# Performance work log

Hardware: AMD Instinct MI355X
Metric: run time of the kernel (lower is better)

## Reference

```python
import jax, jax.numpy as jnp
import numpy as np

R, D, H, NLAYERS = 128, 64, 64, 3
B, N = 64, 1024
INIT_W = 0.1


def setup_inputs() -> dict:
    key = jax.random.key(0)
    ks = jax.random.split(key, 10)
    x = jax.random.normal(ks[0], (B, D, N), dtype=jnp.float32)
    L = jax.random.randint(ks[1], (B, 1, N), 0, 2, dtype=jnp.int32)
    wq0 = INIT_W * jax.random.normal(ks[2], (R, D), dtype=jnp.float32)
    wqr = INIT_W * jax.random.normal(ks[3], (NLAYERS - 1, R, R), dtype=jnp.float32)
    wk0 = INIT_W * jax.random.normal(ks[4], (R, D), dtype=jnp.float32)
    wkr = INIT_W * jax.random.normal(ks[5], (NLAYERS - 1, R, R), dtype=jnp.float32)
    wv0 = INIT_W * jax.random.normal(ks[6], (R, D), dtype=jnp.float32)
    wvr = INIT_W * jax.random.normal(ks[7], (NLAYERS - 1, R, R), dtype=jnp.float32)
    wor = INIT_W * jax.random.normal(ks[8], (NLAYERS - 1, R, R), dtype=jnp.float32)
    wo_last = INIT_W * jax.random.normal(ks[9], (H, R), dtype=jnp.float32)
    return {"x": x, "L": L, "wq0": wq0, "wqr": wqr, "wk0": wk0, "wkr": wkr,
            "wv0": wv0, "wvr": wvr, "wor": wor, "wo_last": wo_last}


def reference(x, L, wq0, wqr, wk0, wkr, wv0, wvr, wor, wo_last):
    # x: [B, d, N]; L: [B, 1, N] neighbor mask (first row used)
    Lrow = L[:, 0, :].astype(jnp.float32)                      # [B, N]
    num_neighbors = jnp.sum((Lrow >= 1).astype(jnp.float32), axis=1)[:, None, None] + 1.0  # [B,1,1]
    scale = jnp.sqrt(num_neighbors)
    mask = Lrow[:, None, :]                                    # [B, 1, N], broadcast over r

    inp = x
    for layer in range(NLAYERS):
        Wq = wq0 if layer == 0 else wqr[layer - 1]
        Wk = wk0 if layer == 0 else wkr[layer - 1]
        Wv = wv0 if layer == 0 else wvr[layer - 1]
        # sigmoid-gated projections: [B, r, N]
        Q = jax.nn.sigmoid(jnp.einsum('rd,bdn->brn', Wq, inp))
        K = jax.nn.sigmoid(jnp.einsum('rd,bdn->brn', Wk, inp))
        V = jax.nn.sigmoid(jnp.einsum('rd,bdn->brn', Wv, inp))
        # degree-scaled softmax attention over agents: scores [B, N, N]
        A = jax.nn.softmax(jnp.einsum('brn,brm->bnm', Q, K) / scale, axis=-1)
        # o[b,r,n] = sum_m A[b,n,m] * V[b,r,m]  -> [B, r, N]
        o = jnp.einsum('bnm,brm->brn', A, V)
        Wo = wor[layer] if layer < NLAYERS - 1 else wo_last
        inp = jax.nn.silu(jnp.einsum('or,brn->bon', Wo, o))
        if layer != NLAYERS - 1:  # remask_bias=True
            inp = mask * inp
    return inp  # [B, h, N]
```

## Files before the change

kernel.cpp:

```cpp
#include <hip/hip_runtime.h>


typedef __bf16 bf16;
typedef bf16 bf16x2 __attribute__((ext_vector_type(2)));
typedef bf16 bf16x4 __attribute__((ext_vector_type(4)));
typedef bf16 bf16x8 __attribute__((ext_vector_type(8)));
typedef float f32x4 __attribute__((ext_vector_type(4)));
typedef float f32x16 __attribute__((ext_vector_type(16)));
typedef unsigned int u32;
typedef u32 u32x4 __attribute__((ext_vector_type(4)));

#define MFMA32(a, b, c) __builtin_amdgcn_mfma_f32_32x32x16_bf16(a, b, c, 0, 0, 0)
#define ZERO16 {0,0,0,0,0,0,0,0,0,0,0,0,0,0,0,0}
#define LOG2E 1.44269504f

__device__ __forceinline__ float fast_exp2(float x) {
  return __builtin_amdgcn_exp2f(x);
}
__device__ __forceinline__ float fast_sigmoid(float x) {
  return __builtin_amdgcn_rcpf(1.0f + fast_exp2(-LOG2E * x));
}
__device__ __forceinline__ u32 cvt_pk_bf16(float lo, float hi) {
  u32 r;
  asm("v_cvt_pk_bf16_f32 %0, %1, %2" : "=v"(r) : "v"(lo), "v"(hi));
  return r;
}
__device__ __forceinline__ void pl32_swap(u32& a, u32& b) {
  asm("v_permlane32_swap_b32 %0, %1" : "+v"(a), "+v"(b));
}
__device__ __forceinline__ void build_frags(const f32x16 v, bf16x8& f0, bf16x8& f1) {
  u32 t0 = cvt_pk_bf16(v[0], v[1]);
  u32 t1 = cvt_pk_bf16(v[2], v[3]);
  u32 t2 = cvt_pk_bf16(v[4], v[5]);
  u32 t3 = cvt_pk_bf16(v[6], v[7]);
  pl32_swap(t0, t2);
  pl32_swap(t1, t3);
  u32x4 a = {t0, t1, t2, t3};
  f0 = __builtin_bit_cast(bf16x8, a);
  u32 s0 = cvt_pk_bf16(v[8], v[9]);
  u32 s1 = cvt_pk_bf16(v[10], v[11]);
  u32 s2 = cvt_pk_bf16(v[12], v[13]);
  u32 s3 = cvt_pk_bf16(v[14], v[15]);
  pl32_swap(s0, s2);
  pl32_swap(s1, s3);
  u32x4 c = {s0, s1, s2, s3};
  f1 = __builtin_bit_cast(bf16x8, c);
}
__device__ __forceinline__ float treesum16(const f32x16 v) {
  float a0 = v[0] + v[1], a1 = v[2] + v[3], a2 = v[4] + v[5], a3 = v[6] + v[7];
  float a4 = v[8] + v[9], a5 = v[10] + v[11], a6 = v[12] + v[13], a7 = v[14] + v[15];
  float b0 = a0 + a1, b1 = a2 + a3, b2 = a4 + a5, b3 = a6 + a7;
  return (b0 + b1) + (b2 + b3);
}

__global__ __launch_bounds__(256) void prep_kernel(
    const int* __restrict__ L,
    const float* __restrict__ wq0, const float* __restrict__ wqr,
    const float* __restrict__ wk0, const float* __restrict__ wkr,
    const float* __restrict__ wv0, const float* __restrict__ wvr,
    const float* __restrict__ wor, const float* __restrict__ wo_last,
    float* __restrict__ scale_inv, float* __restrict__ biasv,
    bf16* __restrict__ wbf) {
  __shared__ int red[256];
  const int blk = blockIdx.x;
  const int tid = threadIdx.x;
  if (blk < 64) {
    int cnt = 0;
    for (int n = tid; n < 1024; n += 256) cnt += (L[blk * 1024 + n] >= 1) ? 1 : 0;
    red[tid] = cnt;
    __syncthreads();
    for (int s = 128; s > 0; s >>= 1) {
      if (tid < s) red[tid] += red[tid + s];
      __syncthreads();
    }
    if (tid == 0) {
      float iv = rsqrtf((float)red[0] + 1.0f);
      scale_inv[blk] = iv;
      biasv[blk] = fmaxf(0.0f, 128.0f * iv * LOG2E - 80.0f);
    }
  } else {
    for (int i = (blk - 64) * 256 + tid; i < 163840; i += 64 * 256) {
      float v;
      if      (i <   8192) v = wq0[i];
      else if (i <  40960) v = wqr[i - 8192];
      else if (i <  49152) v = wk0[i - 40960];
      else if (i <  81920) v = wkr[i - 49152];
      else if (i <  90112) v = wv0[i - 81920];
      else if (i < 122880) v = wvr[i - 90112];
      else if (i < 155648) v = wor[i - 122880];
      else                 v = wo_last[i - 155648];
      wbf[i] = (bf16)v;
    }
  }
}

__global__ __launch_bounds__(256) void xk0_kernel(
    const float* __restrict__ x, const bf16* __restrict__ Wk,
    const bf16* __restrict__ Wv, bf16* __restrict__ xT,
    bf16* __restrict__ Kt, bf16* __restrict__ Vn) {
  __shared__ float tile[64][65];
  __shared__ __attribute__((aligned(16))) bf16 inp_lds[64 * 72];
  const int tid = threadIdx.x;
  const int lane = tid & 63, wv = tid >> 6;
  const int la = lane & 31, hi = lane >> 5;
  const int b = blockIdx.x >> 4;
  const int t0 = (blockIdx.x & 15) * 64;

  {
    const int nl = tid & 63, dbase = (tid >> 6) * 16;
#pragma unroll
    for (int i = 0; i < 16; i++) {
      int d = dbase + i;
      tile[d][nl] = x[(size_t)(b * 64 + d) * 1024 + t0 + nl];
    }
  }
  __syncthreads();
  {
    const int dl = (tid & 31) * 2, nb = (tid >> 5) * 8;
#pragma unroll
    for (int i = 0; i < 8; i++) {
      int n = nb + i;
      bf16x2 pr = {(bf16)tile[dl][n], (bf16)tile[dl + 1][n]};
      *(bf16x2*)(xT + (size_t)(b * 1024 + t0 + n) * 64 + dl) = pr;
      *(bf16x2*)&inp_lds[n * 72 + dl] = pr;
    }
  }
  __syncthreads();

  const int sub = wv & 1;
  if (wv < 2) {
#pragma unroll
    for (int rt2 = 0; rt2 < 2; rt2++) {
      const int rt = 2 * sub + rt2;
      bf16x8 wf[4];
#pragma unroll
      for (int ks = 0; ks < 4; ks++)
        wf[ks] = *(const bf16x8*)(Wk + (size_t)(la + 32 * rt) * 64 + hi * 8 + ks * 16);
#pragma unroll
      for (int tt = 0; tt < 2; tt++) {
        f32x16 acc = ZERO16;
#pragma unroll
        for (int ks = 0; ks < 4; ks++) {
          bf16x8 bfr = *(const bf16x8*)&inp_lds[(la + 32 * tt) * 72 + hi * 8 + ks * 16];
          acc = MFMA32(wf[ks], bfr, acc);
        }
#pragma unroll
        for (int g = 0; g < 4; g++) {
          bf16x4 pk;
#pragma unroll
          for (int i = 0; i < 4; i++) pk[i] = (bf16)fast_sigmoid(acc[4 * g + i]);
          *(bf16x4*)(Kt + (size_t)(b * 1024 + t0 + 32 * tt + la) * 128 +
                     32 * rt + 8 * g + 4 * hi) = pk;
        }
      }
    }
  } else {
#pragma unroll
    for (int rc2 = 0; rc2 < 2; rc2++) {
      const int rc = 2 * sub + rc2;
      bf16x8 wf[4];
#pragma unroll
      for (int ks = 0; ks < 4; ks++)
        wf[ks] = *(const bf16x8*)(Wv + (size_t)(la + 32 * rc) * 64 + hi * 8 + ks * 16);
#pragma unroll
      for (int tt = 0; tt < 2; tt++) {
        f32x16 acc = ZERO16;
#pragma unroll
        for (int ks = 0; ks < 4; ks++) {
          bf16x8 afr = *(const bf16x8*)&inp_lds[(la + 32 * tt) * 72 + hi * 8 + ks * 16];
          acc = MFMA32(afr, wf[ks], acc);
        }
#pragma unroll
        for (int g = 0; g < 4; g++) {
          bf16x4 pk;
#pragma unroll
          for (int i = 0; i < 4; i++) pk[i] = (bf16)fast_sigmoid(acc[4 * g + i]);
          *(bf16x4*)(Vn + (size_t)(b * 128 + la + 32 * rc) * 1024 +
                     t0 + 32 * tt + 8 * g + 4 * hi) = pk;
        }
      }
    }
  }
}

template <int DIN>
__global__ __launch_bounds__(256) void kv_kernel(
    const bf16* __restrict__ inpT, const bf16* __restrict__ Wk,
    const bf16* __restrict__ Wv, bf16* __restrict__ Kt,
    bf16* __restrict__ Vn) {
  constexpr int SIN = DIN + 8;
  constexpr int KS = DIN / 16;
  constexpr int CPR = DIN / 8;
  __shared__ __attribute__((aligned(16))) bf16 inp_lds[64 * SIN];
  const int tid = threadIdx.x;
  const int lane = tid & 63, wv = tid >> 6;
  const int la = lane & 31, hi = lane >> 5;
  const int b = blockIdx.x >> 4;
  const int t0 = (blockIdx.x & 15) * 64;

  for (int i = tid; i < 64 * CPR; i += 256) {
    int row = i / CPR, c = i % CPR;
    *(bf16x8*)&inp_lds[row * SIN + c * 8] =
        *(const bf16x8*)(inpT + (size_t)(b * 1024 + t0 + row) * DIN + c * 8);
  }
  __syncthreads();

  const int sub = wv & 1;
  if (wv < 2) {
#pragma unroll
    for (int rt2 = 0; rt2 < 2; rt2++) {
      const int rt = 2 * sub + rt2;
      bf16x8 wf[KS];
#pragma unroll
      for (int ks = 0; ks < KS; ks++)
        wf[ks] = *(const bf16x8*)(Wk + (size_t)(la + 32 * rt) * DIN + hi * 8 + ks * 16);
#pragma unroll
      for (int tt = 0; tt < 2; tt++) {
        f32x16 acc = ZERO16;
#pragma unroll
        for (int ks = 0; ks < KS; ks++) {
          bf16x8 bfr = *(const bf16x8*)&inp_lds[(la + 32 * tt) * SIN + hi * 8 + ks * 16];
          acc = MFMA32(wf[ks], bfr, acc);
        }
#pragma unroll
        for (int g = 0; g < 4; g++) {
          bf16x4 pk;
#pragma unroll
          for (int i = 0; i < 4; i++) pk[i] = (bf16)fast_sigmoid(acc[4 * g + i]);
          *(bf16x4*)(Kt + (size_t)(b * 1024 + t0 + 32 * tt + la) * 128 +
                     32 * rt + 8 * g + 4 * hi) = pk;
        }
      }
    }
  } else {
#pragma unroll
    for (int rc2 = 0; rc2 < 2; rc2++) {
      const int rc = 2 * sub + rc2;
      bf16x8 wf[KS];
#pragma unroll
      for (int ks = 0; ks < KS; ks++)
        wf[ks] = *(const bf16x8*)(Wv + (size_t)(la + 32 * rc) * DIN + hi * 8 + ks * 16);
#pragma unroll
      for (int tt = 0; tt < 2; tt++) {
        f32x16 acc = ZERO16;
#pragma unroll
        for (int ks = 0; ks < KS; ks++) {
          bf16x8 afr = *(const bf16x8*)&inp_lds[(la + 32 * tt) * SIN + hi * 8 + ks * 16];
          acc = MFMA32(afr, wf[ks], acc);
        }
#pragma unroll
        for (int g = 0; g < 4; g++) {
          bf16x4 pk;
#pragma unroll
          for (int i = 0; i < 4; i++) pk[i] = (bf16)fast_sigmoid(acc[4 * g + i]);
          *(bf16x4*)(Vn + (size_t)(b * 128 + 32 * rc + la) * 1024 +
                     t0 + 32 * tt + 8 * g + 4 * hi) = pk;
        }
      }
    }
  }
}

template <int DIN>
__global__ __launch_bounds__(256, 2) void flash_kernel(
    const bf16* __restrict__ inpT, const bf16* __restrict__ Wq,
    const bf16* __restrict__ Kt, const bf16* __restrict__ Vn,
    const float* __restrict__ scale_inv, const float* __restrict__ biasv,
    const int* __restrict__ L, const bf16* __restrict__ Wo,
    void* __restrict__ outp, int last,
    const bf16* __restrict__ Wkn, const bf16* __restrict__ Wvn,
    bf16* __restrict__ Ktn, bf16* __restrict__ Vnn, int kvgen) {
  __shared__ __attribute__((aligned(16))) char smem[71680];

  const int tid = threadIdx.x;
  const int lane = tid & 63, wv = tid >> 6;
  const int la = lane & 31, hi = lane >> 5;
  const int xcd = blockIdx.x & 7;
  const int kk = blockIdx.x >> 3;
  const int b = xcd * 8 + (kk & 7);
  const int q0 = (kk >> 3) * 128;

  const float inv2 = scale_inv[b] * LOG2E;
  const float bb = biasv[b];

  const int krow = tid >> 4, kc = (tid & 15) * 8;
  const int vrow = tid >> 3, vc = (tid & 7) * 8;
  const bf16* kbase = Kt + (size_t)b * 1024 * 128;
  const bf16* vbase = Vn + (size_t)b * 128 * 1024;

  bf16x8 kr[4], vr[4];
#pragma unroll
  for (int p = 0; p < 4; p++) {
    kr[p] = *(const bf16x8*)(kbase + (size_t)(krow + 16 * p) * 128 + kc);
    vr[p] = *(const bf16x8*)(vbase + (size_t)(vrow + 32 * p) * 1024 + vc);
  }

  bf16x8 qB[8];
  {
    constexpr int SIN = DIN + 8;
    constexpr int KSD = DIN / 16;
    constexpr int CPR = DIN / 8;
    bf16* inp_s = (bf16*)smem;
    for (int i = tid; i < 128 * CPR; i += 256) {
      int row = i / CPR, c = i % CPR;
      *(bf16x8*)&inp_s[row * SIN + c * 8] =
          *(const bf16x8*)(inpT + (size_t)(b * 1024 + q0 + row) * DIN + c * 8);
    }
    __syncthreads();
    bf16x8 bfr[KSD];
#pragma unroll
    for (int ks = 0; ks < KSD; ks++)
      bfr[ks] = *(const bf16x8*)&inp_s[(32 * wv + la) * SIN + hi * 8 + ks * 16];
#pragma unroll
    for (int rt = 0; rt < 4; rt++) {
      f32x16 acc = ZERO16;
#pragma unroll
      for (int ks = 0; ks < KSD; ks++) {
        bf16x8 wf = *(const bf16x8*)(Wq + (size_t)(32 * rt + la) * DIN +
                                     hi * 8 + ks * 16);
        acc = MFMA32(wf, bfr[ks], acc);
      }
      f32x16 qv;
#pragma unroll
      for (int j = 0; j < 16; j++) qv[j] = fast_sigmoid(acc[j]) * inv2;
      build_frags(qv, qB[2 * rt], qB[2 * rt + 1]);
    }
    __syncthreads();
  }

  {
    bf16* K0 = (bf16*)smem;
    bf16* V0 = (bf16*)(smem + 34816);
#pragma unroll
    for (int p = 0; p < 4; p++) *(bf16x8*)&K0[(krow + 16 * p) * 136 + kc] = kr[p];
#pragma unroll
    for (int p = 0; p < 4; p++) *(bf16x8*)&V0[(vrow + 32 * p) * 72 + vc] = vr[p];
#pragma unroll
    for (int p = 0; p < 4; p++) {
      kr[p] = *(const bf16x8*)(kbase + (size_t)(64 + krow + 16 * p) * 128 + kc);
      vr[p] = *(const bf16x8*)(vbase + (size_t)(vrow + 32 * p) * 1024 + 64 + vc);
    }
    __syncthreads();
  }

  f32x16 acc_o[4] = {ZERO16, ZERO16, ZERO16, ZERO16};
  float rs = 0.f;

  for (int it = 0; it < 16; it++) {
    const int cur = it & 1;
    const bf16* Kc = (const bf16*)(smem + cur * 17408);
    const bf16* Vc = (const bf16*)(smem + 34816 + cur * 18432);
    if (it < 15) {
      bf16* Kn = (bf16*)(smem + (1 - cur) * 17408);
      bf16* Vx = (bf16*)(smem + 34816 + (1 - cur) * 18432);
#pragma unroll
      for (int p = 0; p < 4; p++)
        *(bf16x8*)&Kn[(krow + 16 * p) * 136 + kc] = kr[p];
#pragma unroll
      for (int p = 0; p < 4; p++)
        *(bf16x8*)&Vx[(vrow + 32 * p) * 72 + vc] = vr[p];
    }
    if (it < 14) {
      const int m2 = (it + 2) * 64;
#pragma unroll
      for (int p = 0; p < 4; p++) {
        kr[p] = *(const bf16x8*)(kbase + (size_t)(m2 + krow + 16 * p) * 128 + kc);
        vr[p] = *(const bf16x8*)(vbase + (size_t)(vrow + 32 * p) * 1024 + m2 + vc);
      }
    }

    f32x16 s00 = ZERO16, s01 = ZERO16, s10 = ZERO16, s11 = ZERO16;
    __builtin_amdgcn_s_setprio(1);
#pragma unroll
    for (int ks = 0; ks < 4; ks++) {
      bf16x8 k0a = *(const bf16x8*)&Kc[la * 136 + hi * 8 + ks * 16];
      s00 = MFMA32(k0a, qB[ks], s00);
      bf16x8 k0b = *(const bf16x8*)&Kc[la * 136 + hi * 8 + (ks + 4) * 16];
      s01 = MFMA32(k0b, qB[ks + 4], s01);
      bf16x8 k1a = *(const bf16x8*)&Kc[(32 + la) * 136 + hi * 8 + ks * 16];
      s10 = MFMA32(k1a, qB[ks], s10);
      bf16x8 k1b = *(const bf16x8*)&Kc[(32 + la) * 136 + hi * 8 + (ks + 4) * 16];
      s11 = MFMA32(k1b, qB[ks + 4], s11);
    }
    __builtin_amdgcn_s_setprio(0);

    bf16x8 pa[4];
    {
      f32x16 pv;
#pragma unroll
      for (int j = 0; j < 16; j++) pv[j] = fast_exp2(s00[j] + s01[j] - bb);
      rs += treesum16(pv);
      build_frags(pv, pa[0], pa[1]);
    }
    {
      f32x16 pv;
#pragma unroll
      for (int j = 0; j < 16; j++) pv[j] = fast_exp2(s10[j] + s11[j] - bb);
      rs += treesum16(pv);
      build_frags(pv, pa[2], pa[3]);
    }

    __builtin_amdgcn_s_setprio(1);
#pragma unroll
    for (int rt = 0; rt < 4; rt++) {
#pragma unroll
      for (int k2 = 0; k2 < 4; k2++) {
        bf16x8 vB = *(const bf16x8*)&Vc[(32 * rt + la) * 72 + hi * 8 + k2 * 16];
        acc_o[rt] = MFMA32(pa[k2], vB, acc_o[rt]);
      }
    }
    __builtin_amdgcn_s_setprio(0);
    __syncthreads();
  }

  rs += __shfl_xor(rs, 32, 64);
  float* rsp = (float*)(smem + 34816);
  if (lane < 32) rsp[32 * wv + la] = rs;
  bf16* O_lds = (bf16*)smem;
#pragma unroll
  for (int g = 0; g < 4; g++) {
    const int qb = 8 * g + 4 * hi;
    f32x4 r4 = *(f32x4*)&rsp[32 * wv + qb];
    f32x4 is;
#pragma unroll
    for (int i = 0; i < 4; i++) is[i] = 1.0f / r4[i];
#pragma unroll
    for (int rt = 0; rt < 4; rt++) {
#pragma unroll
      for (int i = 0; i < 4; i++) {
        O_lds[(size_t)(32 * wv + qb + i) * 136 + 32 * rt + la] =
            (bf16)(acc_o[rt][4 * g + i] * is[i]);
      }
    }
  }
  __syncthreads();

  if (!last) {
    bf16* out_b = (bf16*)outp;
    bf16* O2 = (bf16*)(smem + 36864);
    const int* Lg = L + b * 1024 + q0;
    bf16x8 wB[8];
#pragma unroll
    for (int ks = 0; ks < 8; ks++)
      wB[ks] = *(const bf16x8*)(Wo + (size_t)(la + 32 * wv) * 128 + hi * 8 + ks * 16);
#pragma unroll
    for (int nt = 0; nt < 4; nt++) {
      f32x16 acc = ZERO16;
#pragma unroll
      for (int ks = 0; ks < 8; ks++) {
        bf16x8 oA = *(const bf16x8*)&O_lds[(size_t)(la + 32 * nt) * 136 +
                                           hi * 8 + ks * 16];
        acc = MFMA32(oA, wB[ks], acc);
      }
#pragma unroll
      for (int g = 0; g < 4; g++) {
#pragma unroll
        for (int i = 0; i < 4; i++) {
          int n = 32 * nt + 8 * g + 4 * hi + i;
          float xv = acc[4 * g + i];
          float y = xv * fast_sigmoid(xv) * (float)Lg[n];
          out_b[(size_t)(b * 1024 + q0 + n) * 128 + 32 * wv + la] = (bf16)y;
          if (kvgen) O2[(size_t)n * 136 + 32 * wv + la] = (bf16)y;
        }
      }
    }
    if (kvgen) {
      __syncthreads();
      const bf16* O2c = (const bf16*)(smem + 36864);
      const int sub = wv & 1;
      const bf16* W2 = (wv < 2) ? Wkn : Wvn;
#pragma unroll
      for (int rt2 = 0; rt2 < 2; rt2++) {
        const int rt = 2 * sub + rt2;
        bf16x8 wf[8];
#pragma unroll
        for (int ks = 0; ks < 8; ks++)
          wf[ks] = *(const bf16x8*)(W2 + (size_t)(la + 32 * rt) * 128 +
                                    hi * 8 + ks * 16);
#pragma unroll
        for (int tt = 0; tt < 4; tt++) {
          f32x16 acc = ZERO16;
          if (wv < 2) {
#pragma unroll
            for (int ks = 0; ks < 8; ks++) {
              bf16x8 bB = *(const bf16x8*)&O2c[(size_t)(32 * tt + la) * 136 +
                                               hi * 8 + ks * 16];
              acc = MFMA32(wf[ks], bB, acc);
            }
#pragma unroll
            for (int g = 0; g < 4; g++) {
              bf16x4 pk;
#pragma unroll
              for (int i = 0; i < 4; i++) pk[i] = (bf16)fast_sigmoid(acc[4 * g + i]);
              *(bf16x4*)(Ktn + (size_t)(b * 1024 + q0 + 32 * tt + la) * 128 +
                         32 * rt + 8 * g + 4 * hi) = pk;
            }
          } else {
#pragma unroll
            for (int ks = 0; ks < 8; ks++) {
              bf16x8 aA = *(const bf16x8*)&O2c[(size_t)(32 * tt + la) * 136 +
                                               hi * 8 + ks * 16];
              acc = MFMA32(aA, wf[ks], acc);
            }
#pragma unroll
            for (int g = 0; g < 4; g++) {
              bf16x4 pk;
#pragma unroll
              for (int i = 0; i < 4; i++) pk[i] = (bf16)fast_sigmoid(acc[4 * g + i]);
              *(bf16x4*)(Vnn + (size_t)(b * 128 + 32 * rt + la) * 1024 +
                         q0 + 32 * tt + 8 * g + 4 * hi) = pk;
            }
          }
        }
      }
    }
  } else {
    const int hs = wv & 1, nq = wv >> 1;
    float* outf = (float*)outp;
    bf16x8 wA[8];
#pragma unroll
    for (int ks = 0; ks < 8; ks++)
      wA[ks] = *(const bf16x8*)(Wo + (size_t)(la + 32 * hs) * 128 + hi * 8 + ks * 16);
#pragma unroll
    for (int t = 0; t < 2; t++) {
      const int ns4 = nq + 2 * t;
      f32x16 acc = ZERO16;
#pragma unroll
      for (int ks = 0; ks < 8; ks++) {
        bf16x8 oB = *(const bf16x8*)&O_lds[(size_t)(32 * ns4 + la) * 136 +
                                           hi * 8 + ks * 16];
        acc = MFMA32(wA[ks], oB, acc);
      }
#pragma unroll
      for (int g = 0; g < 4; g++) {
#pragma unroll
        for (int i = 0; i < 4; i++) {
          int h = 32 * hs + 8 * g + 4 * hi + i;
          float xv = acc[4 * g + i];
          outf[(size_t)(b * 64 + h) * 1024 + q0 + 32 * ns4 + la] =
              xv * fast_sigmoid(xv);
        }
      }
    }
  }
}

__global__ __launch_bounds__(256) void xpose_kernel(const float* __restrict__ x,
                                                    bf16* __restrict__ xT) {
  __shared__ float tile[64][65];
  const int blk = blockIdx.x;
  const int b = blk >> 4;
  const int n0 = (blk & 15) * 64;
  const int tid = threadIdx.x;
  {
    const int nl = tid & 63, dbase = (tid >> 6) * 16;
#pragma unroll
    for (int i = 0; i < 16; i++) {
      int d = dbase + i;
      tile[d][nl] = x[(size_t)(b * 64 + d) * 1024 + n0 + nl];
    }
  }
  __syncthreads();
  {
    const int dl = (tid & 31) * 2, nb = (tid >> 5) * 8;
#pragma unroll
    for (int i = 0; i < 8; i++) {
      int n = nb + i;
      bf16x2 pr = {(bf16)tile[dl][n], (bf16)tile[dl + 1][n]};
      *(bf16x2*)(xT + (size_t)(b * 1024 + n0 + n) * 64 + dl) = pr;
    }
  }
}

extern "C" void kernel_launch(void* const* d_in, const int* in_sizes, int n_in,
                              void* d_out, int out_size, void* d_ws, size_t ws_size,
                              hipStream_t stream) {
  const float* x = (const float*)d_in[0];
  const int* L = (const int*)d_in[1];
  const float* wq0 = (const float*)d_in[2];
  const float* wqr = (const float*)d_in[3];
  const float* wk0 = (const float*)d_in[4];
  const float* wkr = (const float*)d_in[5];
  const float* wv0 = (const float*)d_in[6];
  const float* wvr = (const float*)d_in[7];
  const float* wor = (const float*)d_in[8];
  const float* wo_last = (const float*)d_in[9];

  char* ws = (char*)d_ws;
  float* scale_inv = (float*)(ws + 0);
  float* biasv = (float*)(ws + 1024);
  bf16* wbf = (bf16*)(ws + 4096);
  bf16* xT = (bf16*)(ws + 335872);
  bf16* inpT = (bf16*)(ws + 8724480);
  bf16* KtA = (bf16*)(ws + 25501696);
  bf16* VnA = (bf16*)(ws + 42278912);
  bf16* KtB = (bf16*)(ws + 59056128);
  bf16* VnB = (bf16*)(ws + 75833344);

  prep_kernel<<<128, 256, 0, stream>>>(L, wq0, wqr, wk0, wkr, wv0, wvr, wor,
                                       wo_last, scale_inv, biasv, wbf);

  if (ws_size >= 92610560) {
    xk0_kernel<<<1024, 256, 0, stream>>>(x, wbf + 40960, wbf + 81920, xT, KtA, VnA);
    flash_kernel<64><<<512, 256, 0, stream>>>(
        xT, wbf + 0, KtA, VnA, scale_inv, biasv, L, wbf + 122880, (void*)inpT, 0,
        wbf + 49152, wbf + 90112, KtB, VnB, 1);
    flash_kernel<128><<<512, 256, 0, stream>>>(
        inpT, wbf + 8192, KtB, VnB, scale_inv, biasv, L, wbf + 139264,
        (void*)inpT, 0, wbf + 65536, wbf + 106496, KtA, VnA, 1);
    flash_kernel<128><<<512, 256, 0, stream>>>(
        inpT, wbf + 24576, KtA, VnA, scale_inv, biasv, L, wbf + 155648, d_out, 1,
        nullptr, nullptr, nullptr, nullptr, 0);
  } else if (ws_size >= 59056128) {
    xpose_kernel<<<1024, 256, 0, stream>>>(x, xT);
    for (int l = 0; l < 3; l++) {
      const bf16* Wq = (l == 0) ? wbf + 0 : wbf + 8192 + (size_t)(l - 1) * 16384;
      const bf16* Wk = (l == 0) ? wbf + 40960 : wbf + 49152 + (size_t)(l - 1) * 16384;
      const bf16* Wv = (l == 0) ? wbf + 81920 : wbf + 90112 + (size_t)(l - 1) * 16384;
      const bf16* Wo = (l < 2) ? wbf + 122880 + (size_t)l * 16384 : wbf + 155648;
      void* outp = (l < 2) ? (void*)inpT : (void*)d_out;
      if (l == 0) {
        kv_kernel<64><<<1024, 256, 0, stream>>>(xT, Wk, Wv, KtA, VnA);
        flash_kernel<64><<<512, 256, 0, stream>>>(xT, Wq, KtA, VnA, scale_inv,
                                                  biasv, L, Wo, outp, 0,
                                                  nullptr, nullptr, nullptr,
                                                  nullptr, 0);
      } else {
        kv_kernel<128><<<1024, 256, 0, stream>>>(inpT, Wk, Wv, KtA, VnA);
        flash_kernel<128><<<512, 256, 0, stream>>>(inpT, Wq, KtA, VnA, scale_inv,
                                                   biasv, L, Wo, outp,
                                                   (l == 2) ? 1 : 0, nullptr,
                                                   nullptr, nullptr, nullptr, 0);
      }
    }
  }
}
```

Baseline: 272.5 us.

## Load K fragments directly from global into registers, bypassing LDS staging

Each wave now reads its K MFMA fragments straight from global memory into registers (kfA/kfB) instead of staging K tiles through double-buffered LDS. The next tile's loads are issued after the softmax step so they overlap with the P·V MFMAs. This removes the LDS writes and reads for K and frees LDS, so the shared-memory regions are remapped and one barrier is dropped. The QK score accumulation is also merged into one 8-deep accumulator chain per row half instead of two split chains. In exchange, all four waves fetch the same K data from global/L2, and about 64 extra VGPRs are needed, which could hurt occupancy.

```diff
diff --git a/kernel.cpp b/kernel.cpp
--- a/kernel.cpp
+++ b/kernel.cpp
@@ -283,24 +283,24 @@
   const float inv2 = scale_inv[b] * LOG2E;
   const float bb = biasv[b];
 
-  const int krow = tid >> 4, kc = (tid & 15) * 8;
   const int vrow = tid >> 3, vc = (tid & 7) * 8;
   const bf16* kbase = Kt + (size_t)b * 1024 * 128;
   const bf16* vbase = Vn + (size_t)b * 128 * 1024;
 
-  bf16x8 kr[4], vr[4];
-#pragma unroll
-  for (int p = 0; p < 4; p++) {
-    kr[p] = *(const bf16x8*)(kbase + (size_t)(krow + 16 * p) * 128 + kc);
+  bf16x8 vr[4];
+#pragma unroll
+  for (int p = 0; p < 4; p++)
     vr[p] = *(const bf16x8*)(vbase + (size_t)(vrow + 32 * p) * 1024 + vc);
-  }
+
+  const bf16* ka0 = kbase + (size_t)la * 128 + hi * 8;
+  const bf16* ka1 = kbase + (size_t)(32 + la) * 128 + hi * 8;
 
   bf16x8 qB[8];
   {
     constexpr int SIN = DIN + 8;
     constexpr int KSD = DIN / 16;
     constexpr int CPR = DIN / 8;
-    bf16* inp_s = (bf16*)smem;
+    bf16* inp_s = (bf16*)(smem + 36864);
     for (int i = tid; i < 128 * CPR; i += 256) {
       int row = i / CPR, c = i % CPR;
       *(bf16x8*)&inp_s[row * SIN + c * 8] =
@@ -325,20 +325,21 @@
       for (int j = 0; j < 16; j++) qv[j] = fast_sigmoid(acc[j]) * inv2;
       build_frags(qv, qB[2 * rt], qB[2 * rt + 1]);
     }
-    __syncthreads();
-  }
-
+  }
+
+  bf16x8 kfA[8], kfB[8];
   {
-    bf16* K0 = (bf16*)smem;
-    bf16* V0 = (bf16*)(smem + 34816);
-#pragma unroll
-    for (int p = 0; p < 4; p++) *(bf16x8*)&K0[(krow + 16 * p) * 136 + kc] = kr[p];
-#pragma unroll
-    for (int p = 0; p < 4; p++) *(bf16x8*)&V0[(vrow + 32 * p) * 72 + vc] = vr[p];
-#pragma unroll
-    for (int p = 0; p < 4; p++) {
-      kr[p] = *(const bf16x8*)(kbase + (size_t)(64 + krow + 16 * p) * 128 + kc);
+    bf16* V0 = (bf16*)smem;
+#pragma unroll
+    for (int p = 0; p < 4; p++)
+      *(bf16x8*)&V0[(vrow + 32 * p) * 72 + vc] = vr[p];
+#pragma unroll
+    for (int p = 0; p < 4; p++)
       vr[p] = *(const bf16x8*)(vbase + (size_t)(vrow + 32 * p) * 1024 + 64 + vc);
+#pragma unroll
+    for (int ks = 0; ks < 8; ks++) {
+      kfA[ks] = *(const bf16x8*)(ka0 + ks * 16);
+      kfB[ks] = *(const bf16x8*)(ka1 + ks * 16);
     }
     __syncthreads();
   }
@@ -348,39 +349,20 @@
 
   for (int it = 0; it < 16; it++) {
     const int cur = it & 1;
-    const bf16* Kc = (const bf16*)(smem + cur * 17408);
-    const bf16* Vc = (const bf16*)(smem + 34816 + cur * 18432);
+    const bf16* Vc = (const bf16*)(smem + cur * 18432);
     if (it < 15) {
-      bf16* Kn = (bf16*)(smem + (1 - cur) * 17408);
-      bf16* Vx = (bf16*)(smem + 34816 + (1 - cur) * 18432);
-#pragma unroll
-      for (int p = 0; p < 4; p++)
-        *(bf16x8*)&Kn[(krow + 16 * p) * 136 + kc] = kr[p];
+      bf16* Vx = (bf16*)(smem + (1 - cur) * 18432);
 #pragma unroll
       for (int p = 0; p < 4; p++)
         *(bf16x8*)&Vx[(vrow + 32 * p) * 72 + vc] = vr[p];
     }
-    if (it < 14) {
-      const int m2 = (it + 2) * 64;
-#pragma unroll
-      for (int p = 0; p < 4; p++) {
-        kr[p] = *(const bf16x8*)(kbase + (size_t)(m2 + krow + 16 * p) * 128 + kc);
-        vr[p] = *(const bf16x8*)(vbase + (size_t)(vrow + 32 * p) * 1024 + m2 + vc);
-      }
-    }
-
-    f32x16 s00 = ZERO16, s01 = ZERO16, s10 = ZERO16, s11 = ZERO16;
+
+    f32x16 sa0 = ZERO16, sa1 = ZERO16;
     __builtin_amdgcn_s_setprio(1);
 #pragma unroll
-    for (int ks = 0; ks < 4; ks++) {
-      bf16x8 k0a = *(const bf16x8*)&Kc[la * 136 + hi * 8 + ks * 16];
-      s00 = MFMA32(k0a, qB[ks], s00);
-      bf16x8 k0b = *(const bf16x8*)&Kc[la * 136 + hi * 8 + (ks + 4) * 16];
-      s01 = MFMA32(k0b, qB[ks + 4], s01);
-      bf16x8 k1a = *(const bf16x8*)&Kc[(32 + la) * 136 + hi * 8 + ks * 16];
-      s10 = MFMA32(k1a, qB[ks], s10);
-      bf16x8 k1b = *(const bf16x8*)&Kc[(32 + la) * 136 + hi * 8 + (ks + 4) * 16];
-      s11 = MFMA32(k1b, qB[ks + 4], s11);
+    for (int ks = 0; ks < 8; ks++) {
+      sa0 = MFMA32(kfA[ks], qB[ks], sa0);
+      sa1 = MFMA32(kfB[ks], qB[ks], sa1);
     }
     __builtin_amdgcn_s_setprio(0);
 
@@ -388,16 +370,32 @@
     {
       f32x16 pv;
 #pragma unroll
-      for (int j = 0; j < 16; j++) pv[j] = fast_exp2(s00[j] + s01[j] - bb);
+      for (int j = 0; j < 16; j++) pv[j] = fast_exp2(sa0[j] - bb);
       rs += treesum16(pv);
       build_frags(pv, pa[0], pa[1]);
     }
     {
       f32x16 pv;
 #pragma unroll
-      for (int j = 0; j < 16; j++) pv[j] = fast_exp2(s10[j] + s11[j] - bb);
+      for (int j = 0; j < 16; j++) pv[j] = fast_exp2(sa1[j] - bb);
       rs += treesum16(pv);
       build_frags(pv, pa[2], pa[3]);
+    }
+
+    if (it < 15) {
+      ka0 += 64 * 128;
+      ka1 += 64 * 128;
+#pragma unroll
+      for (int ks = 0; ks < 8; ks++) {
+        kfA[ks] = *(const bf16x8*)(ka0 + ks * 16);
+        kfB[ks] = *(const bf16x8*)(ka1 + ks * 16);
+      }
+    }
+    if (it < 14) {
+      const int m2 = (it + 2) * 64;
+#pragma unroll
+      for (int p = 0; p < 4; p++)
+        vr[p] = *(const bf16x8*)(vbase + (size_t)(vrow + 32 * p) * 1024 + m2 + vc);
     }
 
     __builtin_amdgcn_s_setprio(1);
@@ -414,9 +412,9 @@
   }
 
   rs += __shfl_xor(rs, 32, 64);
-  float* rsp = (float*)(smem + 34816);
+  float* rsp = (float*)smem;
   if (lane < 32) rsp[32 * wv + la] = rs;
-  bf16* O_lds = (bf16*)smem;
+  bf16* O_lds = (bf16*)(smem + 36864);
 #pragma unroll
   for (int g = 0; g < 4; g++) {
     const int qb = 8 * g + 4 * hi;
@@ -437,7 +435,7 @@
 
   if (!last) {
     bf16* out_b = (bf16*)outp;
-    bf16* O2 = (bf16*)(smem + 36864);
+    bf16* O2 = (bf16*)(smem + 1024);
     const int* Lg = L + b * 1024 + q0;
     bf16x8 wB[8];
 #pragma unroll
@@ -466,7 +464,7 @@
     }
     if (kvgen) {
       __syncthreads();
-      const bf16* O2c = (const bf16*)(smem + 36864);
+      const bf16* O2c = (const bf16*)(smem + 1024);
       const int sub = wv & 1;
       const bf16* W2 = (wv < 2) ? Wkn : Wvn;
 #pragma unroll
```

After: 366.0 us. +34.3%, slower.

## Stage K/V tiles via direct global-to-LDS loads with XOR-swizzled layout

Applied to the files above, without the earlier changes.

Replaces the register-staged K/V prefetch (global load to VGPRs, then LDS store) with global_load_lds 16-byte direct copies into double-buffered LDS tiles. Padded row strides are replaced by an XOR swizzle on 16-byte chunks to avoid bank conflicts, and the reads are adjusted to match. This frees VGPRs and removes the LDS store instructions. The prefetch distance drops from two tiles to one, which could expose more load latency, and it relies on the barrier to cover the async LDS writes.

```diff
diff --git a/kernel.cpp b/kernel.cpp
--- a/kernel.cpp
+++ b/kernel.cpp
@@ -51,6 +51,11 @@
   float a4 = v[8] + v[9], a5 = v[10] + v[11], a6 = v[12] + v[13], a7 = v[14] + v[15];
   float b0 = a0 + a1, b1 = a2 + a3, b2 = a4 + a5, b3 = a6 + a7;
   return (b0 + b1) + (b2 + b3);
+}
+__device__ __forceinline__ void gload16(const bf16* g, char* lds) {
+  __builtin_amdgcn_global_load_lds(
+      (const __attribute__((address_space(1))) void*)g,
+      (__attribute__((address_space(3))) void*)lds, 16, 0, 0);
 }
 
 __global__ __launch_bounds__(256) void prep_kernel(
@@ -282,18 +287,31 @@
 
   const float inv2 = scale_inv[b] * LOG2E;
   const float bb = biasv[b];
-
-  const int krow = tid >> 4, kc = (tid & 15) * 8;
-  const int vrow = tid >> 3, vc = (tid & 7) * 8;
+  const int sw = la & 7;
+
   const bf16* kbase = Kt + (size_t)b * 1024 * 128;
   const bf16* vbase = Vn + (size_t)b * 128 * 1024;
 
-  bf16x8 kr[4], vr[4];
-#pragma unroll
-  for (int p = 0; p < 4; p++) {
-    kr[p] = *(const bf16x8*)(kbase + (size_t)(krow + 16 * p) * 128 + kc);
-    vr[p] = *(const bf16x8*)(vbase + (size_t)(vrow + 32 * p) * 1024 + vc);
-  }
+  auto stage_tile = [&](int tok0, char* kd, char* vd) {
+#pragma unroll
+    for (int c = 0; c < 4; c++) {
+      const int reg = wv * 4 + c;
+      {
+        const int row = reg * 4 + (lane >> 4);
+        const int slot = lane & 15;
+        const bf16* src = kbase + (size_t)(tok0 + row) * 128 +
+                          (((slot & 7) ^ (row & 7) | (slot & 8)) << 3);
+        gload16(src, kd + reg * 1024);
+      }
+      {
+        const int row = reg * 8 + (lane >> 3);
+        const int slot = lane & 7;
+        const bf16* src = vbase + (size_t)row * 1024 + tok0 +
+                          ((slot ^ (row & 7)) << 3);
+        gload16(src, vd + reg * 1024);
+      }
+    }
+  };
 
   bf16x8 qB[8];
   {
@@ -328,58 +346,34 @@
     __syncthreads();
   }
 
-  {
-    bf16* K0 = (bf16*)smem;
-    bf16* V0 = (bf16*)(smem + 34816);
-#pragma unroll
-    for (int p = 0; p < 4; p++) *(bf16x8*)&K0[(krow + 16 * p) * 136 + kc] = kr[p];
-#pragma unroll
-    for (int p = 0; p < 4; p++) *(bf16x8*)&V0[(vrow + 32 * p) * 72 + vc] = vr[p];
-#pragma unroll
-    for (int p = 0; p < 4; p++) {
-      kr[p] = *(const bf16x8*)(kbase + (size_t)(64 + krow + 16 * p) * 128 + kc);
-      vr[p] = *(const bf16x8*)(vbase + (size_t)(vrow + 32 * p) * 1024 + 64 + vc);
-    }
-    __syncthreads();
-  }
+  stage_tile(0, smem, smem + 32768);
+  __syncthreads();
 
   f32x16 acc_o[4] = {ZERO16, ZERO16, ZERO16, ZERO16};
   float rs = 0.f;
 
   for (int it = 0; it < 16; it++) {
     const int cur = it & 1;
-    const bf16* Kc = (const bf16*)(smem + cur * 17408);
-    const bf16* Vc = (const bf16*)(smem + 34816 + cur * 18432);
-    if (it < 15) {
-      bf16* Kn = (bf16*)(smem + (1 - cur) * 17408);
-      bf16* Vx = (bf16*)(smem + 34816 + (1 - cur) * 18432);
-#pragma unroll
-      for (int p = 0; p < 4; p++)
-        *(bf16x8*)&Kn[(krow + 16 * p) * 136 + kc] = kr[p];
-#pragma unroll
-      for (int p = 0; p < 4; p++)
-        *(bf16x8*)&Vx[(vrow + 32 * p) * 72 + vc] = vr[p];
-    }
-    if (it < 14) {
-      const int m2 = (it + 2) * 64;
-#pragma unroll
-      for (int p = 0; p < 4; p++) {
-        kr[p] = *(const bf16x8*)(kbase + (size_t)(m2 + krow + 16 * p) * 128 + kc);
-        vr[p] = *(const bf16x8*)(vbase + (size_t)(vrow + 32 * p) * 1024 + m2 + vc);
-      }
-    }
+    const bf16* Kc = (const bf16*)(smem + cur * 16384);
+    const bf16* Vc = (const bf16*)(smem + 32768 + cur * 16384);
+    if (it < 15)
+      stage_tile((it + 1) * 64, smem + (1 - cur) * 16384,
+                 smem + 32768 + (1 - cur) * 16384);
 
     f32x16 s00 = ZERO16, s01 = ZERO16, s10 = ZERO16, s11 = ZERO16;
     __builtin_amdgcn_s_setprio(1);
 #pragma unroll
     for (int ks = 0; ks < 4; ks++) {
-      bf16x8 k0a = *(const bf16x8*)&Kc[la * 136 + hi * 8 + ks * 16];
+      bf16x8 k0a = *(const bf16x8*)&Kc[(size_t)la * 128 + (((hi + 2 * ks) ^ sw) << 3)];
       s00 = MFMA32(k0a, qB[ks], s00);
-      bf16x8 k0b = *(const bf16x8*)&Kc[la * 136 + hi * 8 + (ks + 4) * 16];
+      bf16x8 k0b = *(const bf16x8*)&Kc[(size_t)la * 128 +
+                                       ((((hi + 2 * (ks + 4)) & 7 ^ sw) | 8) << 3)];
       s01 = MFMA32(k0b, qB[ks + 4], s01);
-      bf16x8 k1a = *(const bf16x8*)&Kc[(32 + la) * 136 + hi * 8 + ks * 16];
+      bf16x8 k1a = *(const bf16x8*)&Kc[(size_t)(32 + la) * 128 +
+                                       (((hi + 2 * ks) ^ sw) << 3)];
       s10 = MFMA32(k1a, qB[ks], s10);
-      bf16x8 k1b = *(const bf16x8*)&Kc[(32 + la) * 136 + hi * 8 + (ks + 4) * 16];
+      bf16x8 k1b = *(const bf16x8*)&Kc[(size_t)(32 + la) * 128 +
+                                       ((((hi + 2 * (ks + 4)) & 7 ^ sw) | 8) << 3)];
       s11 = MFMA32(k1b, qB[ks + 4], s11);
     }
     __builtin_amdgcn_s_setprio(0);
@@ -405,7 +399,8 @@
     for (int rt = 0; rt < 4; rt++) {
 #pragma unroll
       for (int k2 = 0; k2 < 4; k2++) {
-        bf16x8 vB = *(const bf16x8*)&Vc[(32 * rt + la) * 72 + hi * 8 + k2 * 16];
+        bf16x8 vB = *(const bf16x8*)&Vc[(size_t)(32 * rt + la) * 64 +
+                                        (((hi + 2 * k2) ^ sw) << 3)];
         acc_o[rt] = MFMA32(pa[k2], vB, acc_o[rt]);
       }
     }
```

Result: no change. 273.1 us (+0.2%).

## Compact unmasked keys and add masked-token attention contribution analytically

Applied to the files above, without the earlier changes.

In layers 1 and 2 every masked token has zero input, so its K and V are the constant sigmoid(0)=0.5. The prep kernel now builds per-chunk prefix counts of unmasked tokens. The KV-generation epilogue scatters K and V for unmasked tokens into a compacted prefix, and pads the tail up to a 64-token tile with K=-128 and V=0. The flash loop then runs only over the compacted tiles, and the masked tokens' softmax mass is added back in closed form from the row sum of Q. This roughly halves attention work in those layers, at the cost of scattered, partly scalar V stores and a slightly different bf16 rounding path.

```diff
diff --git a/kernel.cpp b/kernel.cpp
--- a/kernel.cpp
+++ b/kernel.cpp
@@ -60,13 +60,20 @@
     const float* __restrict__ wv0, const float* __restrict__ wvr,
     const float* __restrict__ wor, const float* __restrict__ wo_last,
     float* __restrict__ scale_inv, float* __restrict__ biasv,
-    bf16* __restrict__ wbf) {
+    int* __restrict__ cinfo, bf16* __restrict__ wbf) {
   __shared__ int red[256];
+  __shared__ int ch[8];
   const int blk = blockIdx.x;
   const int tid = threadIdx.x;
   if (blk < 64) {
+    if (tid < 8) ch[tid] = 0;
+    __syncthreads();
     int cnt = 0;
-    for (int n = tid; n < 1024; n += 256) cnt += (L[blk * 1024 + n] >= 1) ? 1 : 0;
+    for (int n = tid; n < 1024; n += 256) {
+      int m = (L[blk * 1024 + n] >= 1) ? 1 : 0;
+      cnt += m;
+      if (m) atomicAdd(&ch[n >> 7], 1);
+    }
     red[tid] = cnt;
     __syncthreads();
     for (int s = 128; s > 0; s >>= 1) {
@@ -77,6 +84,12 @@
       float iv = rsqrtf((float)red[0] + 1.0f);
       scale_inv[blk] = iv;
       biasv[blk] = fmaxf(0.0f, 128.0f * iv * LOG2E - 80.0f);
+      int run = 0;
+      for (int c = 0; c < 8; c++) {
+        cinfo[blk * 9 + c] = run;
+        run += ch[c];
+      }
+      cinfo[blk * 9 + 8] = run;
     }
   } else {
     for (int i = (blk - 64) * 256 + tid; i < 163840; i += 64 * 256) {
@@ -269,7 +282,8 @@
     const int* __restrict__ L, const bf16* __restrict__ Wo,
     void* __restrict__ outp, int last,
     const bf16* __restrict__ Wkn, const bf16* __restrict__ Wvn,
-    bf16* __restrict__ Ktn, bf16* __restrict__ Vnn, int kvgen) {
+    bf16* __restrict__ Ktn, bf16* __restrict__ Vnn, int kvgen,
+    const int* __restrict__ cinfo, int cin) {
   __shared__ __attribute__((aligned(16))) char smem[71680];
 
   const int tid = threadIdx.x;
@@ -282,6 +296,11 @@
 
   const float inv2 = scale_inv[b] * LOG2E;
   const float bb = biasv[b];
+  const int* ci = cinfo + b * 9;
+  const int cntU = ci[8];
+  const int presq = ci[q0 >> 7];
+  const int nt = cin ? ((cntU + 63) >> 6) : 16;
+  const int cm = 1024 - cntU;
 
   const int krow = tid >> 4, kc = (tid & 15) * 8;
   const int vrow = tid >> 3, vc = (tid & 7) * 8;
@@ -296,6 +315,7 @@
   }
 
   bf16x8 qB[8];
+  float sq = 0.f;
   {
     constexpr int SIN = DIN + 8;
     constexpr int KSD = DIN / 16;
@@ -323,8 +343,15 @@
       f32x16 qv;
 #pragma unroll
       for (int j = 0; j < 16; j++) qv[j] = fast_sigmoid(acc[j]) * inv2;
+      if (cin) {
+        float s = 0.f;
+#pragma unroll
+        for (int j = 0; j < 16; j++) s += (float)(bf16)qv[j];
+        sq += s;
+      }
       build_frags(qv, qB[2 * rt], qB[2 * rt + 1]);
     }
+    sq += __shfl_xor(sq, 32, 64);
     __syncthreads();
   }
 
@@ -346,11 +373,11 @@
   f32x16 acc_o[4] = {ZERO16, ZERO16, ZERO16, ZERO16};
   float rs = 0.f;
 
-  for (int it = 0; it < 16; it++) {
+  for (int it = 0; it < nt; it++) {
     const int cur = it & 1;
     const bf16* Kc = (const bf16*)(smem + cur * 17408);
     const bf16* Vc = (const bf16*)(smem + 34816 + cur * 18432);
-    if (it < 15) {
+    if (it < nt - 1) {
       bf16* Kn = (bf16*)(smem + (1 - cur) * 17408);
       bf16* Vx = (bf16*)(smem + 34816 + (1 - cur) * 18432);
 #pragma unroll
@@ -360,7 +387,7 @@
       for (int p = 0; p < 4; p++)
         *(bf16x8*)&Vx[(vrow + 32 * p) * 72 + vc] = vr[p];
     }
-    if (it < 14) {
+    if (it < nt - 2) {
       const int m2 = (it + 2) * 64;
 #pragma unroll
       for (int p = 0; p < 4; p++) {
@@ -414,6 +441,21 @@
   }
 
   rs += __shfl_xor(rs, 32, 64);
+  if (cin) {
+    rs += (float)cm * fast_exp2(0.5f * sq - bb);
+    const float hc = 0.5f * (float)cm;
+#pragma unroll
+    for (int j = 0; j < 16; j++) {
+      const int qrow = (j & 3) + 8 * (j >> 2) + 4 * hi;
+      float sj = __shfl(sq, qrow, 64);
+      float add = hc * fast_exp2(0.5f * sj - bb);
+      acc_o[0][j] += add;
+      acc_o[1][j] += add;
+      acc_o[2][j] += add;
+      acc_o[3][j] += add;
+    }
+  }
+
   float* rsp = (float*)(smem + 34816);
   if (lane < 32) rsp[32 * wv + la] = rs;
   bf16* O_lds = (bf16*)smem;
@@ -444,11 +486,11 @@
     for (int ks = 0; ks < 8; ks++)
       wB[ks] = *(const bf16x8*)(Wo + (size_t)(la + 32 * wv) * 128 + hi * 8 + ks * 16);
 #pragma unroll
-    for (int nt = 0; nt < 4; nt++) {
+    for (int nt2 = 0; nt2 < 4; nt2++) {
       f32x16 acc = ZERO16;
 #pragma unroll
       for (int ks = 0; ks < 8; ks++) {
-        bf16x8 oA = *(const bf16x8*)&O_lds[(size_t)(la + 32 * nt) * 136 +
+        bf16x8 oA = *(const bf16x8*)&O_lds[(size_t)(la + 32 * nt2) * 136 +
                                            hi * 8 + ks * 16];
         acc = MFMA32(oA, wB[ks], acc);
       }
@@ -456,7 +498,7 @@
       for (int g = 0; g < 4; g++) {
 #pragma unroll
         for (int i = 0; i < 4; i++) {
-          int n = 32 * nt + 8 * g + 4 * hi + i;
+          int n = 32 * nt2 + 8 * g + 4 * hi + i;
           float xv = acc[4 * g + i];
           float y = xv * fast_sigmoid(xv) * (float)Lg[n];
           out_b[(size_t)(b * 1024 + q0 + n) * 128 + 32 * wv + la] = (bf16)y;
@@ -466,49 +508,100 @@
     }
     if (kvgen) {
       __syncthreads();
+      int* dl = (int*)(smem + 35328);
+      int* cc = (int*)(smem + 35840);
+      if (tid < 128) {
+        int m = (Lg[tid] != 0) ? 1 : 0;
+        unsigned long long bal = __ballot(m);
+        int ex = (int)__popcll(bal & ((1ull << lane) - 1));
+        if (lane == 0) cc[wv] = (int)__popcll(bal);
+        dl[tid] = (m << 16) | ex;
+      }
+      __syncthreads();
+      if (tid < 128) {
+        int t = dl[tid];
+        int m = t >> 16, ex = t & 0xffff;
+        if (wv == 1) ex += cc[0];
+        dl[tid] = m ? (presq + ex)
+                    : ~(cntU + (q0 - presq) + (tid - ex));
+      }
+      __syncthreads();
+      const int slots = ((cntU + 63) >> 6) << 6;
       const bf16* O2c = (const bf16*)(smem + 36864);
       const int sub = wv & 1;
-      const bf16* W2 = (wv < 2) ? Wkn : Wvn;
-#pragma unroll
-      for (int rt2 = 0; rt2 < 2; rt2++) {
-        const int rt = 2 * sub + rt2;
-        bf16x8 wf[8];
-#pragma unroll
-        for (int ks = 0; ks < 8; ks++)
-          wf[ks] = *(const bf16x8*)(W2 + (size_t)(la + 32 * rt) * 128 +
-                                    hi * 8 + ks * 16);
-#pragma unroll
-        for (int tt = 0; tt < 4; tt++) {
-          f32x16 acc = ZERO16;
-          if (wv < 2) {
+      if (wv < 2) {
+        const bf16* W2 = Wkn;
+#pragma unroll
+        for (int rt2 = 0; rt2 < 2; rt2++) {
+          const int rt = 2 * sub + rt2;
+          bf16x8 wf[8];
+#pragma unroll
+          for (int ks = 0; ks < 8; ks++)
+            wf[ks] = *(const bf16x8*)(W2 + (size_t)(la + 32 * rt) * 128 +
+                                      hi * 8 + ks * 16);
+#pragma unroll
+          for (int tt = 0; tt < 4; tt++) {
+            f32x16 acc = ZERO16;
 #pragma unroll
             for (int ks = 0; ks < 8; ks++) {
               bf16x8 bB = *(const bf16x8*)&O2c[(size_t)(32 * tt + la) * 136 +
                                                hi * 8 + ks * 16];
               acc = MFMA32(wf[ks], bB, acc);
             }
+            const int e = dl[32 * tt + la];
 #pragma unroll
             for (int g = 0; g < 4; g++) {
               bf16x4 pk;
 #pragma unroll
               for (int i = 0; i < 4; i++) pk[i] = (bf16)fast_sigmoid(acc[4 * g + i]);
-              *(bf16x4*)(Ktn + (size_t)(b * 1024 + q0 + 32 * tt + la) * 128 +
-                         32 * rt + 8 * g + 4 * hi) = pk;
+              if (e >= 0) {
+                *(bf16x4*)(Ktn + (size_t)(b * 1024 + e) * 128 +
+                           32 * rt + 8 * g + 4 * hi) = pk;
+              } else {
+                int dm = ~e;
+                if (dm < slots) {
+                  bf16x4 sv = {(bf16)-128.f, (bf16)-128.f, (bf16)-128.f,
+                               (bf16)-128.f};
+                  *(bf16x4*)(Ktn + (size_t)(b * 1024 + dm) * 128 +
+                             32 * rt + 8 * g + 4 * hi) = sv;
+                }
+              }
             }
-          } else {
+          }
+        }
+      } else {
+        const bf16* W2 = Wvn;
+#pragma unroll
+        for (int rt2 = 0; rt2 < 2; rt2++) {
+          const int rt = 2 * sub + rt2;
+          bf16x8 wf[8];
+#pragma unroll
+          for (int ks = 0; ks < 8; ks++)
+            wf[ks] = *(const bf16x8*)(W2 + (size_t)(la + 32 * rt) * 128 +
+                                      hi * 8 + ks * 16);
+#pragma unroll
+          for (int tt = 0; tt < 4; tt++) {
+            f32x16 acc = ZERO16;
 #pragma unroll
             for (int ks = 0; ks < 8; ks++) {
               bf16x8 aA = *(const bf16x8*)&O2c[(size_t)(32 * tt + la) * 136 +
                                                hi * 8 + ks * 16];
               acc = MFMA32(aA, wf[ks], acc);
             }
+            bf16* vrow_p = Vnn + (size_t)(b * 128 + 32 * rt + la) * 1024;
 #pragma unroll
             for (int g = 0; g < 4; g++) {
-              bf16x4 pk;
-#pragma unroll
-              for (int i = 0; i < 4; i++) pk[i] = (bf16)fast_sigmoid(acc[4 * g + i]);
-              *(bf16x4*)(Vnn + (size_t)(b * 128 + 32 * rt + la) * 1024 +
-                         q0 + 32 * tt + 8 * g + 4 * hi) = pk;
+#pragma unroll
+              for (int i = 0; i < 4; i++) {
+                const int tok = 32 * tt + 8 * g + 4 * hi + i;
+                const int e = dl[tok];
+                if (e >= 0) {
+                  vrow_p[e] = (bf16)fast_sigmoid(acc[4 * g + i]);
+                } else {
+                  int dm = ~e;
+                  if (dm < slots) vrow_p[dm] = (bf16)0.f;
+                }
+              }
             }
           }
         }
@@ -589,6 +682,7 @@
   char* ws = (char*)d_ws;
   float* scale_inv = (float*)(ws + 0);
   float* biasv = (float*)(ws + 1024);
+  int* cinfo = (int*)(ws + 1536);
   bf16* wbf = (bf16*)(ws + 4096);
   bf16* xT = (bf16*)(ws + 335872);
   bf16* inpT = (bf16*)(ws + 8724480);
@@ -598,19 +692,19 @@
   bf16* VnB = (bf16*)(ws + 75833344);
 
   prep_kernel<<<128, 256, 0, stream>>>(L, wq0, wqr, wk0, wkr, wv0, wvr, wor,
-                                       wo_last, scale_inv, biasv, wbf);
+                                       wo_last, scale_inv, biasv, cinfo, wbf);
 
   if (ws_size >= 92610560) {
     xk0_kernel<<<1024, 256, 0, stream>>>(x, wbf + 40960, wbf + 81920, xT, KtA, VnA);
     flash_kernel<64><<<512, 256, 0, stream>>>(
         xT, wbf + 0, KtA, VnA, scale_inv, biasv, L, wbf + 122880, (void*)inpT, 0,
-        wbf + 49152, wbf + 90112, KtB, VnB, 1);
+        wbf + 49152, wbf + 90112, KtB, VnB, 1, cinfo, 0);
     flash_kernel<128><<<512, 256, 0, stream>>>(
         inpT, wbf + 8192, KtB, VnB, scale_inv, biasv, L, wbf + 139264,
-        (void*)inpT, 0, wbf + 65536, wbf + 106496, KtA, VnA, 1);
+        (void*)inpT, 0, wbf + 65536, wbf + 106496, KtA, VnA, 1, cinfo, 1);
     flash_kernel<128><<<512, 256, 0, stream>>>(
         inpT, wbf + 24576, KtA, VnA, scale_inv, biasv, L, wbf + 155648, d_out, 1,
-        nullptr, nullptr, nullptr, nullptr, 0);
+        nullptr, nullptr, nullptr, nullptr, 0, cinfo, 1);
   } else if (ws_size >= 59056128) {
     xpose_kernel<<<1024, 256, 0, stream>>>(x, xT);
     for (int l = 0; l < 3; l++) {
@@ -624,14 +718,15 @@
         flash_kernel<64><<<512, 256, 0, stream>>>(xT, Wq, KtA, VnA, scale_inv,
                                                   biasv, L, Wo, outp, 0,
                                                   nullptr, nullptr, nullptr,
-                                                  nullptr, 0);
+                                                  nullptr, 0, cinfo, 0);
       } else {
         kv_kernel<128><<<1024, 256, 0, stream>>>(inpT, Wk, Wv, KtA, VnA);
         flash_kernel<128><<<512, 256, 0, stream>>>(inpT, Wq, KtA, VnA, scale_inv,
                                                    biasv, L, Wo, outp,
                                                    (l == 2) ? 1 : 0, nullptr,
-                                                   nullptr, nullptr, nullptr, 0);
-      }
-    }
-  }
-}
+                                                   nullptr, nullptr, nullptr, 0,
+                                                   cinfo, 0);
+      }
+    }
+  }
+}
```

After: 274.3 us. No clear change (+0.7%).
